# Kernel tuning notes

Hardware: AMD Instinct MI355X
Metric: run time of the kernel (lower is better)

## Reference

```python
import jax, jax.numpy as jnp
import numpy as np

B, CQ, CK, CV, CO = 16, 256, 256, 256, 256
H, W = 80, 80          # query spatial size (P3-like)
KH, KW = 40, 40        # key/value spatial size (P4-like)
HEADS = 4
R2 = 2 * 2             # region_size ** 2
SCALE = 1.0 / np.float32(np.sqrt(CQ))


def conv1x1(x, w, b):
    # 1x1 conv == per-pixel linear map over channels
    return jnp.einsum('bchw,oc->bohw', x, w) + b[None, :, None, None]


def setup_inputs() -> dict:
    key = jax.random.key(0)
    ks = jax.random.split(key, 10)
    s = 0.05
    return {
        'query': jax.random.normal(ks[0], (B, CQ, H, W), jnp.float32),
        'key':   jax.random.normal(ks[1], (B, CK, KH, KW), jnp.float32),
        'wq': jax.random.normal(ks[2], (CQ, CQ), jnp.float32) * s,
        'bq': jax.random.normal(ks[3], (CQ,), jnp.float32) * s,
        'wk': jax.random.normal(ks[4], (CK, CK), jnp.float32) * s,
        'bk': jax.random.normal(ks[5], (CK,), jnp.float32) * s,
        'wv': jax.random.normal(ks[6], (CV, CV), jnp.float32) * s,
        'bv': jax.random.normal(ks[7], (CV,), jnp.float32) * s,
        'wo': jax.random.normal(ks[8], (CO, CV), jnp.float32) * s,
        'bo': jax.random.normal(ks[9], (CO,), jnp.float32) * s,
    }


def reference(query, key, wq, bq, wk, bk, wv, bv, wo, bo):
    # value defaults to key in the original module
    q = conv1x1(query, wq, bq)               # [B,CQ,H,W]
    k = conv1x1(key, wk, bk)                 # [B,CK,KH,KW]
    v = conv1x1(key, wv, bv)                 # [B,CV,KH,KW]

    b, cq, h, w = q.shape
    # All R2 'patches' in the source are the SAME interpolation (no offsets),
    # so compute it once; bilinear resize matches torch align_corners=False.
    ki = jax.image.resize(k, (b, k.shape[1], h, w), method='bilinear')
    vi = jax.image.resize(v, (b, v.shape[1], h, w), method='bilinear')

    q5 = q.reshape(b, HEADS, cq // HEADS, h, w)
    k5 = ki.reshape(b, HEADS, k.shape[1] // HEADS, h, w)
    v5 = vi.reshape(b, HEADS, v.shape[1] // HEADS, h, w)

    # per-region score; identical for every region patch
    score = jnp.einsum('bhcxy,bhcxy->bhxy', q5, k5) * SCALE     # [B,h,H,W]
    scores = jnp.broadcast_to(score[:, :, None], (b, HEADS, R2, h, w))
    # NOTE: original uses nn.Softmax(dim=3) -> normalizes over the H axis
    attn = jax.nn.softmax(scores, axis=3)                       # [B,h,R2,H,W]

    # out = sum over regions of attn * v (v identical across regions)
    out = jnp.einsum('bhrxy,bhcxy->bhcxy', attn, v5)            # [B,h,C/h,H,W]
    out = out.reshape(b, -1, h, w)                              # [B,CV,H,W]
    return conv1x1(out, wo, bo)                                 # [B,CO,H,W]
```

## Files before the change

### kernel.cpp

```cpp
#include <hip/hip_runtime.h>
#include <hip/hip_bf16.h>

typedef __bf16 bf16;
typedef __attribute__((ext_vector_type(4))) float f32x4;
typedef __attribute__((ext_vector_type(8))) __bf16 bf16x8;
typedef __attribute__((ext_vector_type(4))) __bf16 bf16x4;

static __device__ __forceinline__ void gl16(const void* g, void* l) {
  __builtin_amdgcn_global_load_lds((const __attribute__((address_space(1))) void*)g,
                                   (__attribute__((address_space(3))) void*)l, 16, 0, 0);
}
static __device__ __forceinline__ bf16x8 frag(const bf16* tile, int row, int kb) {
  return *(const bf16x8*)(tile + row * 64 + ((((kb) >> 3) ^ (row & 7)) << 3));
}

__global__ void wpre(const float* __restrict__ w0, const float* __restrict__ w1,
                     const float* __restrict__ w2, const float* __restrict__ w3,
                     bf16* __restrict__ dst) {
  const float* srcs[4] = {w0, w1, w2, w3};
  const float* s = srcs[blockIdx.y];
  bf16* d = dst + (size_t)blockIdx.y * 65536;
  int base = blockIdx.x * 2048 + threadIdx.x * 8;
  f32x4 a = *(const f32x4*)(s + base);
  f32x4 b = *(const f32x4*)(s + base + 4);
  bf16x8 v = {(bf16)a[0], (bf16)a[1], (bf16)a[2], (bf16)a[3],
              (bf16)b[0], (bf16)b[1], (bf16)b[2], (bf16)b[3]};
  *(bf16x8*)(d + base) = v;
}

__global__ __launch_bounds__(256, 1)
void qscore(const float* __restrict__ query, const bf16* __restrict__ Wq,
            const float* __restrict__ bq, const bf16* __restrict__ Kpm,
            float* __restrict__ score) {
  __shared__ alignas(16) char smem[64 * 264 * 2];
  const int t = threadIdx.x;
  const int b = blockIdx.z;
  const int p0 = blockIdx.x * 64;
  const int w = t >> 6, l = t & 63;
  const int lrow = l & 15, ksel = l >> 4;
  const int pq = t & 15, cq = t >> 4;
  const float* actb = query + (size_t)b * 256 * 6400;
  bf16* As = (bf16*)smem;

  f32x4 Ar[4][4];
#pragma unroll
  for (int kt = 0; kt < 4; ++kt)
#pragma unroll
    for (int j = 0; j < 4; ++j)
      Ar[kt][j] = *(const f32x4*)(actb + (size_t)(kt * 64 + cq * 4 + j) * 6400 + p0 + pq * 4);
#pragma unroll
  for (int kt = 0; kt < 4; ++kt) {
    bf16* tile = As + kt * 4096;
#pragma unroll
    for (int e = 0; e < 4; ++e) {
      int row = pq * 4 + e;
      bf16x4 v = {(bf16)Ar[kt][0][e], (bf16)Ar[kt][1][e], (bf16)Ar[kt][2][e], (bf16)Ar[kt][3][e]};
      *(bf16x4*)(tile + row * 64 + ((((cq >> 1) ^ (row & 7)) << 3) | ((cq & 1) << 2))) = v;
    }
  }
  __syncthreads();

  f32x4 acc[4][4];
#pragma unroll
  for (int i = 0; i < 4; ++i)
#pragma unroll
    for (int j = 0; j < 4; ++j) acc[i][j] = (f32x4){0.f, 0.f, 0.f, 0.f};

#pragma unroll
  for (int kt = 0; kt < 4; ++kt) {
    const int k0 = kt * 64;
    const bf16* tile = As + kt * 4096;
    bf16x8 af[4][2], bv[4][2];
#pragma unroll
    for (int mi = 0; mi < 4; ++mi)
#pragma unroll
      for (int kk = 0; kk < 2; ++kk)
        af[mi][kk] = *(const bf16x8*)(Wq + (size_t)(w * 64 + mi * 16 + lrow) * 256 +
                                      k0 + kk * 32 + ksel * 8);
#pragma unroll
    for (int ni = 0; ni < 4; ++ni)
#pragma unroll
      for (int kk = 0; kk < 2; ++kk)
        bv[ni][kk] = frag(tile, ni * 16 + lrow, kk * 32 + ksel * 8);
#pragma unroll
    for (int kk = 0; kk < 2; ++kk)
#pragma unroll
      for (int mi = 0; mi < 4; ++mi)
#pragma unroll
        for (int ni = 0; ni < 4; ++ni)
          acc[mi][ni] = __builtin_amdgcn_mfma_f32_16x16x32_bf16(af[mi][kk], bv[ni][kk],
                                                                acc[mi][ni], 0, 0, 0);
  }
  __syncthreads();

  bf16* Qs = (bf16*)smem;
#pragma unroll
  for (int mi = 0; mi < 4; ++mi) {
#pragma unroll
    for (int r = 0; r < 4; ++r) {
      int o = w * 64 + mi * 16 + ksel * 4 + r;
      float bvf = bq[o];
#pragma unroll
      for (int ni = 0; ni < 4; ++ni) {
        int px = ni * 16 + lrow;
        Qs[px * 264 + o] = (bf16)(acc[mi][ni][r] + bvf);
      }
    }
  }
  __syncthreads();

  {
    int pl = t & 63, hd = t >> 6;
    int p = p0 + pl;
    int x = p / 80, y = p % 80;
    float cx = 0.5f * x - 0.25f;
    int ix = (int)floorf(cx);
    float wx1 = cx - ix;
    int x0 = ix < 0 ? 0 : ix, x1 = (ix + 1 > 39) ? 39 : ix + 1;
    float cy = 0.5f * y - 0.25f;
    int iy = (int)floorf(cy);
    float wy1 = cy - iy;
    int y0 = iy < 0 ? 0 : iy, y1 = (iy + 1 > 39) ? 39 : iy + 1;
    float w00 = (1.f - wx1) * (1.f - wy1), w01 = (1.f - wx1) * wy1;
    float w10 = wx1 * (1.f - wy1), w11 = wx1 * wy1;
    const bf16* k00 = Kpm + ((size_t)b * 1600 + x0 * 40 + y0) * 256 + hd * 64;
    const bf16* k01 = Kpm + ((size_t)b * 1600 + x0 * 40 + y1) * 256 + hd * 64;
    const bf16* k10 = Kpm + ((size_t)b * 1600 + x1 * 40 + y0) * 256 + hd * 64;
    const bf16* k11 = Kpm + ((size_t)b * 1600 + x1 * 40 + y1) * 256 + hd * 64;
    float dot = 0.f;
#pragma unroll
    for (int i = 0; i < 8; ++i) {
      bf16x8 qv = *(const bf16x8*)(Qs + pl * 264 + hd * 64 + i * 8);
      bf16x8 a = *(const bf16x8*)(k00 + i * 8);
      bf16x8 c = *(const bf16x8*)(k01 + i * 8);
      bf16x8 d = *(const bf16x8*)(k10 + i * 8);
      bf16x8 e = *(const bf16x8*)(k11 + i * 8);
#pragma unroll
      for (int j = 0; j < 8; ++j) {
        float kup = w00 * (float)a[j] + w01 * (float)c[j] + w10 * (float)d[j] + w11 * (float)e[j];
        dot += (float)qv[j] * kup;
      }
    }
    score[((size_t)b * 4 + hd) * 6400 + p] = dot * 0.0625f;
  }
}

__global__ __launch_bounds__(256, 1)
void kv_proj(const float* __restrict__ key,
             const bf16* __restrict__ Wk, const float* __restrict__ bk, bf16* __restrict__ Kpm,
             const bf16* __restrict__ Wv, const float* __restrict__ bv, bf16* __restrict__ Vpm) {
  __shared__ alignas(16) char smem[64 * 264 * 2];
  const int P = 1600;
  const int t = threadIdx.x;
  const int b = blockIdx.z;
  const int p0 = blockIdx.x * 64;
  const int sel = blockIdx.y;
  const bf16* W = sel ? Wv : Wk;
  const float* bias = sel ? bv : bk;
  bf16* out = sel ? Vpm : Kpm;
  const int w = t >> 6, l = t & 63;
  const int lrow = l & 15, ksel = l >> 4;
  const int pq = t & 15, cq = t >> 4;
  const float* actb = key + (size_t)b * 256 * P;
  bf16* As = (bf16*)smem;

  f32x4 Ar[4][4];
#pragma unroll
  for (int kt = 0; kt < 4; ++kt)
#pragma unroll
    for (int j = 0; j < 4; ++j)
      Ar[kt][j] = *(const f32x4*)(actb + (size_t)(kt * 64 + cq * 4 + j) * P + p0 + pq * 4);
#pragma unroll
  for (int kt = 0; kt < 4; ++kt) {
    bf16* tile = As + kt * 4096;
#pragma unroll
    for (int e = 0; e < 4; ++e) {
      int row = pq * 4 + e;
      bf16x4 v = {(bf16)Ar[kt][0][e], (bf16)Ar[kt][1][e], (bf16)Ar[kt][2][e], (bf16)Ar[kt][3][e]};
      *(bf16x4*)(tile + row * 64 + ((((cq >> 1) ^ (row & 7)) << 3) | ((cq & 1) << 2))) = v;
    }
  }
  __syncthreads();

  f32x4 acc[4][4];
#pragma unroll
  for (int i = 0; i < 4; ++i)
#pragma unroll
    for (int j = 0; j < 4; ++j) acc[i][j] = (f32x4){0.f, 0.f, 0.f, 0.f};

#pragma unroll
  for (int kt = 0; kt < 4; ++kt) {
    const int k0 = kt * 64;
    const bf16* tile = As + kt * 4096;
    bf16x8 af[4][2], bv8[4][2];
#pragma unroll
    for (int mi = 0; mi < 4; ++mi)
#pragma unroll
      for (int kk = 0; kk < 2; ++kk)
        af[mi][kk] = *(const bf16x8*)(W + (size_t)(w * 64 + mi * 16 + lrow) * 256 +
                                      k0 + kk * 32 + ksel * 8);
#pragma unroll
    for (int ni = 0; ni < 4; ++ni)
#pragma unroll
      for (int kk = 0; kk < 2; ++kk)
        bv8[ni][kk] = frag(tile, ni * 16 + lrow, kk * 32 + ksel * 8);
#pragma unroll
    for (int kk = 0; kk < 2; ++kk)
#pragma unroll
      for (int mi = 0; mi < 4; ++mi)
#pragma unroll
        for (int ni = 0; ni < 4; ++ni)
          acc[mi][ni] = __builtin_amdgcn_mfma_f32_16x16x32_bf16(af[mi][kk], bv8[ni][kk],
                                                                acc[mi][ni], 0, 0, 0);
  }
  __syncthreads();

  bf16* Sc = (bf16*)smem;
#pragma unroll
  for (int mi = 0; mi < 4; ++mi) {
#pragma unroll
    for (int r = 0; r < 4; ++r) {
      int o = w * 64 + mi * 16 + ksel * 4 + r;
      float bvf = bias[o];
#pragma unroll
      for (int ni = 0; ni < 4; ++ni) {
        int px = ni * 16 + lrow;
        Sc[px * 264 + o] = (bf16)(acc[mi][ni][r] + bvf);
      }
    }
  }
  __syncthreads();
  bf16* ob = out + (size_t)b * P * 256 + (size_t)p0 * 256;
#pragma unroll
  for (int pass = 0; pass < 8; ++pass) {
    int idx = pass * 256 + t;
    int row = idx >> 5, cu = idx & 31;
    bf16x8 v = *(const bf16x8*)(Sc + row * 264 + cu * 8);
    *(bf16x8*)(ob + (size_t)row * 256 + cu * 8) = v;
  }
}

__global__ void smax_kernel(float* __restrict__ score) {
  __shared__ float s[6400];
  const int hd = blockIdx.x, b = blockIdx.y, t = threadIdx.x;
  float* buf = score + ((size_t)b * 4 + hd) * 6400;
  for (int i = t; i < 6400; i += 256) s[i] = buf[i];
  __syncthreads();
  if (t < 80) {
    const int y = t;
    float m = -1e30f;
    for (int x = 0; x < 80; ++x) m = fmaxf(m, s[x * 80 + y]);
    float sum = 0.f;
    for (int x = 0; x < 80; ++x) {
      float e = __expf(s[x * 80 + y] - m);
      s[x * 80 + y] = e;
      sum += e;
    }
    float inv = 4.0f / sum;
    for (int x = 0; x < 80; ++x) buf[x * 80 + y] = s[x * 80 + y] * inv;
  }
}

__global__ __launch_bounds__(256, 4)
void uv_gemm(const bf16* __restrict__ Vpm, const bf16* __restrict__ Wo,
             bf16* __restrict__ Uv) {
  __shared__ alignas(16) bf16 Vt[64 * 64];
  const int t = threadIdx.x;
  const int b = blockIdx.z;
  const int hd = blockIdx.y;
  const int q0 = blockIdx.x * 64;
  const int w = t >> 6, l = t & 63;
  const int lrow = l & 15, ksel = l >> 4;

  const bf16* vsrc = Vpm + ((size_t)b * 1600 + q0) * 256 + hd * 64;
#pragma unroll
  for (int call = 0; call < 2; ++call) {
    int idx = (w * 2 + call) * 64 + l;
    int q = idx >> 3, u = idx & 7;
    gl16(vsrc + (size_t)q * 256 + ((u ^ (q & 7)) << 3), Vt + idx * 8);
  }
  asm volatile("s_waitcnt vmcnt(0)" ::: "memory");
  __syncthreads();

  f32x4 acc[4][4];
#pragma unroll
  for (int i = 0; i < 4; ++i)
#pragma unroll
    for (int j = 0; j < 4; ++j) acc[i][j] = (f32x4){0.f, 0.f, 0.f, 0.f};

#pragma unroll
  for (int kk = 0; kk < 2; ++kk) {
    bf16x8 af[4], bv[4];
#pragma unroll
    for (int mi = 0; mi < 4; ++mi)
      af[mi] = *(const bf16x8*)(Wo + (size_t)(w * 64 + mi * 16 + lrow) * 256 +
                                hd * 64 + kk * 32 + ksel * 8);
#pragma unroll
    for (int ni = 0; ni < 4; ++ni)
      bv[ni] = frag(Vt, ni * 16 + lrow, kk * 32 + ksel * 8);
#pragma unroll
    for (int mi = 0; mi < 4; ++mi)
#pragma unroll
      for (int ni = 0; ni < 4; ++ni)
        acc[mi][ni] = __builtin_amdgcn_mfma_f32_16x16x32_bf16(af[mi], bv[ni], acc[mi][ni], 0, 0, 0);
  }

  bf16* ob = Uv + ((size_t)(b * 4 + hd)) * 256 * 1600;
#pragma unroll
  for (int mi = 0; mi < 4; ++mi) {
#pragma unroll
    for (int ni = 0; ni < 4; ++ni) {
#pragma unroll
      for (int r = 0; r < 4; ++r) {
        int o = w * 64 + mi * 16 + ksel * 4 + r;
        int q = q0 + ni * 16 + lrow;
        ob[(size_t)o * 1600 + q] = (bf16)acc[mi][ni][r];
      }
    }
  }
}

__global__ __launch_bounds__(256, 8)
void combine(const bf16* __restrict__ Uv, const float* __restrict__ attn,
             const float* __restrict__ bo, float* __restrict__ out) {
  __shared__ bf16 Us[4][1600];
  __shared__ int   sx0[80], sx1[80];
  __shared__ float swx[80];
  const int t = threadIdx.x;
  const int o = blockIdx.x;
  const int b = blockIdx.y;

  const bf16* usrc = Uv + (size_t)(b * 4) * 256 * 1600 + (size_t)o * 1600;
  for (int idx = t; idx < 800; idx += 256) {
    int hd = idx / 200, u = idx % 200;
    *(bf16x8*)&Us[hd][u * 8] = *(const bf16x8*)(usrc + (size_t)hd * 256 * 1600 + u * 8);
  }
  if (t < 80) {
    float c = 0.5f * t - 0.25f;
    int i0 = (int)floorf(c);
    swx[t] = c - i0;
    sx0[t] = i0 < 0 ? 0 : i0;
    sx1[t] = (i0 + 1 > 39) ? 39 : i0 + 1;
  }
  __syncthreads();

  const float bias = bo[o];
  const float* attb = attn + (size_t)b * 4 * 6400;
  float* op = out + ((size_t)b * 256 + o) * 6400;

  for (int p = t; p < 6400; p += 256) {
    int x = p / 80, y = p - x * 80;
    int x0 = sx0[x], x1 = sx1[x], y0 = sx0[y], y1 = sx1[y];
    float wx1 = swx[x], wy1 = swx[y];
    float w00 = (1.f - wx1) * (1.f - wy1), w01 = (1.f - wx1) * wy1;
    float w10 = wx1 * (1.f - wy1), w11 = wx1 * wy1;
    int q00 = x0 * 40 + y0, q01 = x0 * 40 + y1, q10 = x1 * 40 + y0, q11 = x1 * 40 + y1;
    float acc = bias;
#pragma unroll
    for (int hd = 0; hd < 4; ++hd) {
      float up = w00 * (float)Us[hd][q00] + w01 * (float)Us[hd][q01] +
                 w10 * (float)Us[hd][q10] + w11 * (float)Us[hd][q11];
      acc += attb[hd * 6400 + p] * up;
    }
    op[p] = acc;
  }
}

extern "C" void kernel_launch(void* const* d_in, const int* in_sizes, int n_in,
                              void* d_out, int out_size, void* d_ws, size_t ws_size,
                              hipStream_t stream) {
  const float* query = (const float*)d_in[0];
  const float* key   = (const float*)d_in[1];
  const float* wq    = (const float*)d_in[2];
  const float* bq    = (const float*)d_in[3];
  const float* wk    = (const float*)d_in[4];
  const float* bk    = (const float*)d_in[5];
  const float* wv    = (const float*)d_in[6];
  const float* bv    = (const float*)d_in[7];
  const float* wo    = (const float*)d_in[8];
  const float* bo    = (const float*)d_in[9];

  char* ws = (char*)d_ws;
  bf16*  Uv    = (bf16*)(ws);
  bf16*  Kpm   = (bf16*)(ws + 52428800);
  bf16*  Vpm   = (bf16*)(ws + 65536000);
  float* score = (float*)(ws + 78643200);
  bf16*  Wb    = (bf16*)(ws + 85196800);
  bf16* wqb = Wb, *wkb = Wb + 65536, *wvb = Wb + 131072, *wob = Wb + 196608;

  wpre<<<dim3(32, 4), 256, 0, stream>>>(wq, wk, wv, wo, Wb);
  kv_proj<<<dim3(25, 2, 16), 256, 0, stream>>>(key, wkb, bk, Kpm, wvb, bv, Vpm);
  qscore<<<dim3(100, 1, 16), 256, 0, stream>>>(query, wqb, bq, Kpm, score);
  smax_kernel<<<dim3(4, 16), 256, 0, stream>>>(score);
  uv_gemm<<<dim3(25, 4, 16), 256, 0, stream>>>(Vpm, wob, Uv);
  combine<<<dim3(256, 16), 256, 0, stream>>>(Uv, score, bo, (float*)d_out);
}
```

Measured before the change: 179.9 us.

## Reassociate query score to project keys through Wq instead of projecting queries

Instead of projecting all 6400 query pixels through Wq and then dotting with upsampled keys, the score is rewritten as query·(Wq^T·K_h) plus bq·K_h. A transposed Wq is multiplied with the 1600-pixel key map, reusing the uv_gemm kernel. A new streaming kernel then reads the raw query and bilinearly interpolates the precomputed per-head key projections, avoiding the large Q GEMM at 6400 pixels. This adds per-head intermediates of 256×1600 per batch, stores temporaries in the output buffer, and computes bilinear taps inside the inner loop.

```diff
diff --git a/kernel.cpp b/kernel.cpp
--- a/kernel.cpp
+++ b/kernel.cpp
@@ -28,120 +28,21 @@
   *(bf16x8*)(d + base) = v;
 }
 
-__global__ __launch_bounds__(256, 1)
-void qscore(const float* __restrict__ query, const bf16* __restrict__ Wq,
-            const float* __restrict__ bq, const bf16* __restrict__ Kpm,
-            float* __restrict__ score) {
-  __shared__ alignas(16) char smem[64 * 264 * 2];
-  const int t = threadIdx.x;
-  const int b = blockIdx.z;
-  const int p0 = blockIdx.x * 64;
-  const int w = t >> 6, l = t & 63;
-  const int lrow = l & 15, ksel = l >> 4;
-  const int pq = t & 15, cq = t >> 4;
-  const float* actb = query + (size_t)b * 256 * 6400;
-  bf16* As = (bf16*)smem;
-
-  f32x4 Ar[4][4];
-#pragma unroll
-  for (int kt = 0; kt < 4; ++kt)
-#pragma unroll
-    for (int j = 0; j < 4; ++j)
-      Ar[kt][j] = *(const f32x4*)(actb + (size_t)(kt * 64 + cq * 4 + j) * 6400 + p0 + pq * 4);
-#pragma unroll
-  for (int kt = 0; kt < 4; ++kt) {
-    bf16* tile = As + kt * 4096;
-#pragma unroll
-    for (int e = 0; e < 4; ++e) {
-      int row = pq * 4 + e;
-      bf16x4 v = {(bf16)Ar[kt][0][e], (bf16)Ar[kt][1][e], (bf16)Ar[kt][2][e], (bf16)Ar[kt][3][e]};
-      *(bf16x4*)(tile + row * 64 + ((((cq >> 1) ^ (row & 7)) << 3) | ((cq & 1) << 2))) = v;
-    }
-  }
-  __syncthreads();
-
-  f32x4 acc[4][4];
-#pragma unroll
-  for (int i = 0; i < 4; ++i)
-#pragma unroll
-    for (int j = 0; j < 4; ++j) acc[i][j] = (f32x4){0.f, 0.f, 0.f, 0.f};
-
-#pragma unroll
-  for (int kt = 0; kt < 4; ++kt) {
-    const int k0 = kt * 64;
-    const bf16* tile = As + kt * 4096;
-    bf16x8 af[4][2], bv[4][2];
-#pragma unroll
-    for (int mi = 0; mi < 4; ++mi)
-#pragma unroll
-      for (int kk = 0; kk < 2; ++kk)
-        af[mi][kk] = *(const bf16x8*)(Wq + (size_t)(w * 64 + mi * 16 + lrow) * 256 +
-                                      k0 + kk * 32 + ksel * 8);
-#pragma unroll
-    for (int ni = 0; ni < 4; ++ni)
-#pragma unroll
-      for (int kk = 0; kk < 2; ++kk)
-        bv[ni][kk] = frag(tile, ni * 16 + lrow, kk * 32 + ksel * 8);
-#pragma unroll
-    for (int kk = 0; kk < 2; ++kk)
-#pragma unroll
-      for (int mi = 0; mi < 4; ++mi)
-#pragma unroll
-        for (int ni = 0; ni < 4; ++ni)
-          acc[mi][ni] = __builtin_amdgcn_mfma_f32_16x16x32_bf16(af[mi][kk], bv[ni][kk],
-                                                                acc[mi][ni], 0, 0, 0);
-  }
-  __syncthreads();
-
-  bf16* Qs = (bf16*)smem;
-#pragma unroll
-  for (int mi = 0; mi < 4; ++mi) {
-#pragma unroll
-    for (int r = 0; r < 4; ++r) {
-      int o = w * 64 + mi * 16 + ksel * 4 + r;
-      float bvf = bq[o];
-#pragma unroll
-      for (int ni = 0; ni < 4; ++ni) {
-        int px = ni * 16 + lrow;
-        Qs[px * 264 + o] = (bf16)(acc[mi][ni][r] + bvf);
-      }
-    }
-  }
-  __syncthreads();
-
-  {
-    int pl = t & 63, hd = t >> 6;
-    int p = p0 + pl;
-    int x = p / 80, y = p % 80;
-    float cx = 0.5f * x - 0.25f;
-    int ix = (int)floorf(cx);
-    float wx1 = cx - ix;
-    int x0 = ix < 0 ? 0 : ix, x1 = (ix + 1 > 39) ? 39 : ix + 1;
-    float cy = 0.5f * y - 0.25f;
-    int iy = (int)floorf(cy);
-    float wy1 = cy - iy;
-    int y0 = iy < 0 ? 0 : iy, y1 = (iy + 1 > 39) ? 39 : iy + 1;
-    float w00 = (1.f - wx1) * (1.f - wy1), w01 = (1.f - wx1) * wy1;
-    float w10 = wx1 * (1.f - wy1), w11 = wx1 * wy1;
-    const bf16* k00 = Kpm + ((size_t)b * 1600 + x0 * 40 + y0) * 256 + hd * 64;
-    const bf16* k01 = Kpm + ((size_t)b * 1600 + x0 * 40 + y1) * 256 + hd * 64;
-    const bf16* k10 = Kpm + ((size_t)b * 1600 + x1 * 40 + y0) * 256 + hd * 64;
-    const bf16* k11 = Kpm + ((size_t)b * 1600 + x1 * 40 + y1) * 256 + hd * 64;
-    float dot = 0.f;
-#pragma unroll
-    for (int i = 0; i < 8; ++i) {
-      bf16x8 qv = *(const bf16x8*)(Qs + pl * 264 + hd * 64 + i * 8);
-      bf16x8 a = *(const bf16x8*)(k00 + i * 8);
-      bf16x8 c = *(const bf16x8*)(k01 + i * 8);
-      bf16x8 d = *(const bf16x8*)(k10 + i * 8);
-      bf16x8 e = *(const bf16x8*)(k11 + i * 8);
-#pragma unroll
-      for (int j = 0; j < 8; ++j) {
-        float kup = w00 * (float)a[j] + w01 * (float)c[j] + w10 * (float)d[j] + w11 * (float)e[j];
-        dot += (float)qv[j] * kup;
-      }
-    }
-    score[((size_t)b * 4 + hd) * 6400 + p] = dot * 0.0625f;
+__global__ void wtr(const float* __restrict__ wq, bf16* __restrict__ wqT) {
+  __shared__ float tl[64][65];
+  const int r0 = blockIdx.x * 64, c0 = blockIdx.y * 64;
+  const int t = threadIdx.x;
+  const int cc = t & 63, rr = t >> 6;
+#pragma unroll
+  for (int i = 0; i < 16; ++i) {
+    int r = i * 4 + rr;
+    tl[r][cc] = wq[(size_t)(r0 + r) * 256 + c0 + cc];
+  }
+  __syncthreads();
+#pragma unroll
+  for (int i = 0; i < 16; ++i) {
+    int r = i * 4 + rr;
+    wqT[(size_t)(c0 + r) * 256 + r0 + cc] = (bf16)tl[cc][r];
   }
 }
 
@@ -240,6 +141,171 @@
   }
 }
 
+__global__ __launch_bounds__(256, 4)
+void uv_gemm(const bf16* __restrict__ Bpm, const bf16* __restrict__ A,
+             bf16* __restrict__ D) {
+  __shared__ alignas(16) bf16 Vt[64 * 64];
+  const int t = threadIdx.x;
+  const int b = blockIdx.z;
+  const int hd = blockIdx.y;
+  const int q0 = blockIdx.x * 64;
+  const int w = t >> 6, l = t & 63;
+  const int lrow = l & 15, ksel = l >> 4;
+
+  const bf16* vsrc = Bpm + ((size_t)b * 1600 + q0) * 256 + hd * 64;
+#pragma unroll
+  for (int call = 0; call < 2; ++call) {
+    int idx = (w * 2 + call) * 64 + l;
+    int q = idx >> 3, u = idx & 7;
+    gl16(vsrc + (size_t)q * 256 + ((u ^ (q & 7)) << 3), Vt + idx * 8);
+  }
+  asm volatile("s_waitcnt vmcnt(0)" ::: "memory");
+  __syncthreads();
+
+  f32x4 acc[4][4];
+#pragma unroll
+  for (int i = 0; i < 4; ++i)
+#pragma unroll
+    for (int j = 0; j < 4; ++j) acc[i][j] = (f32x4){0.f, 0.f, 0.f, 0.f};
+
+#pragma unroll
+  for (int kk = 0; kk < 2; ++kk) {
+    bf16x8 af[4], bv[4];
+#pragma unroll
+    for (int mi = 0; mi < 4; ++mi)
+      af[mi] = *(const bf16x8*)(A + (size_t)(w * 64 + mi * 16 + lrow) * 256 +
+                                hd * 64 + kk * 32 + ksel * 8);
+#pragma unroll
+    for (int ni = 0; ni < 4; ++ni)
+      bv[ni] = frag(Vt, ni * 16 + lrow, kk * 32 + ksel * 8);
+#pragma unroll
+    for (int mi = 0; mi < 4; ++mi)
+#pragma unroll
+      for (int ni = 0; ni < 4; ++ni)
+        acc[mi][ni] = __builtin_amdgcn_mfma_f32_16x16x32_bf16(af[mi], bv[ni], acc[mi][ni], 0, 0, 0);
+  }
+
+  bf16* ob = D + ((size_t)(b * 4 + hd)) * 256 * 1600;
+#pragma unroll
+  for (int mi = 0; mi < 4; ++mi) {
+#pragma unroll
+    for (int ni = 0; ni < 4; ++ni) {
+#pragma unroll
+      for (int r = 0; r < 4; ++r) {
+        int o = w * 64 + mi * 16 + ksel * 4 + r;
+        int q = q0 + ni * 16 + lrow;
+        ob[(size_t)o * 1600 + q] = (bf16)acc[mi][ni][r];
+      }
+    }
+  }
+}
+
+__global__ void beta_k(const bf16* __restrict__ Kpm, const float* __restrict__ bq,
+                       bf16* __restrict__ beta) {
+  __shared__ float bqs[256];
+  const int t = threadIdx.x;
+  bqs[t] = bq[t];
+  __syncthreads();
+  const int b = blockIdx.y;
+  const int q = blockIdx.x * 64 + (t >> 2);
+  const int hd = t & 3;
+  const bf16* row = Kpm + ((size_t)b * 1600 + q) * 256 + hd * 64;
+  float s = 0.f;
+#pragma unroll
+  for (int i = 0; i < 8; ++i) {
+    bf16x8 v = *(const bf16x8*)(row + i * 8);
+#pragma unroll
+    for (int j = 0; j < 8; ++j) s += (float)v[j] * bqs[hd * 64 + i * 8 + j];
+  }
+  beta[((size_t)b * 4 + hd) * 1600 + q] = (bf16)s;
+}
+
+__global__ __launch_bounds__(256, 3)
+void stream_score(const float* __restrict__ query, const bf16* __restrict__ T,
+                  const bf16* __restrict__ beta, float* __restrict__ score) {
+  __shared__ alignas(16) bf16 Tc[2][64][192];
+  __shared__ bf16 Bs[4][192];
+  const int t = threadIdx.x;
+  const int p0 = blockIdx.x * 256;
+  const int b = blockIdx.y;
+  const int px = p0 + t;
+  const int x = px / 80, y = px % 80;
+
+  const int x_min = p0 / 80;
+  int ixm = (int)floorf(0.5f * x_min - 0.25f);
+  int xr0 = ixm < 0 ? 0 : ixm;
+  int qbase = xr0 * 40;
+  if (qbase > 1408) qbase = 1408;
+
+  float cx = 0.5f * x - 0.25f;
+  int ix = (int)floorf(cx);
+  float wx1 = cx - ix;
+  int x0 = ix < 0 ? 0 : ix, x1 = (ix + 1 > 39) ? 39 : ix + 1;
+  float cy = 0.5f * y - 0.25f;
+  int iy = (int)floorf(cy);
+  float wy1 = cy - iy;
+  int y0 = iy < 0 ? 0 : iy, y1 = (iy + 1 > 39) ? 39 : iy + 1;
+  const float w00 = (1.f - wx1) * (1.f - wy1), w01 = (1.f - wx1) * wy1;
+  const float w10 = wx1 * (1.f - wy1), w11 = wx1 * wy1;
+  const int r00 = x0 * 40 + y0 - qbase, r01 = x0 * 40 + y1 - qbase;
+  const int r10 = x1 * 40 + y0 - qbase, r11 = x1 * 40 + y1 - qbase;
+
+  for (int i = t; i < 768; i += 256) {
+    int hd = i / 192, qq = i - hd * 192;
+    Bs[hd][qq] = beta[((size_t)b * 4 + hd) * 1600 + qbase + qq];
+  }
+
+  const bf16* Tb = T + (size_t)b * 4 * 256 * 1600;
+
+  auto STAGE = [&](int c, int buf) {
+    const int k0 = c * 16;
+#pragma unroll
+    for (int call = 0; call < 6; ++call) {
+      int idx = call * 256 + t;
+      int r = idx / 24, u = idx - r * 24;
+      int hd = r >> 4, kk = r & 15;
+      const bf16* src = Tb + ((size_t)(hd * 256) + k0 + kk) * 1600 + qbase + u * 8;
+      gl16(src, &Tc[buf][0][0] + idx * 8);
+    }
+  };
+
+  STAGE(0, 0);
+  asm volatile("s_waitcnt vmcnt(0)" ::: "memory");
+  __syncthreads();
+
+  float acc[4];
+#pragma unroll
+  for (int hd = 0; hd < 4; ++hd)
+    acc[hd] = w00 * (float)Bs[hd][r00] + w01 * (float)Bs[hd][r01] +
+              w10 * (float)Bs[hd][r10] + w11 * (float)Bs[hd][r11];
+
+  int buf = 0;
+  for (int c = 0; c < 16; ++c) {
+    if (c < 15) STAGE(c + 1, buf ^ 1);
+    float qv[16];
+#pragma unroll
+    for (int kk = 0; kk < 16; ++kk)
+      qv[kk] = query[((size_t)b * 256 + c * 16 + kk) * 6400 + px];
+#pragma unroll
+    for (int kk = 0; kk < 16; ++kk) {
+#pragma unroll
+      for (int hd = 0; hd < 4; ++hd) {
+        const bf16* row = &Tc[buf][hd * 16 + kk][0];
+        float tv = w00 * (float)row[r00] + w01 * (float)row[r01] +
+                   w10 * (float)row[r10] + w11 * (float)row[r11];
+        acc[hd] += qv[kk] * tv;
+      }
+    }
+    asm volatile("s_waitcnt vmcnt(0)" ::: "memory");
+    __syncthreads();
+    buf ^= 1;
+  }
+
+#pragma unroll
+  for (int hd = 0; hd < 4; ++hd)
+    score[((size_t)b * 4 + hd) * 6400 + px] = 0.0625f * acc[hd];
+}
+
 __global__ void smax_kernel(float* __restrict__ score) {
   __shared__ float s[6400];
   const int hd = blockIdx.x, b = blockIdx.y, t = threadIdx.x;
@@ -258,65 +324,6 @@
     }
     float inv = 4.0f / sum;
     for (int x = 0; x < 80; ++x) buf[x * 80 + y] = s[x * 80 + y] * inv;
-  }
-}
-
-__global__ __launch_bounds__(256, 4)
-void uv_gemm(const bf16* __restrict__ Vpm, const bf16* __restrict__ Wo,
-             bf16* __restrict__ Uv) {
-  __shared__ alignas(16) bf16 Vt[64 * 64];
-  const int t = threadIdx.x;
-  const int b = blockIdx.z;
-  const int hd = blockIdx.y;
-  const int q0 = blockIdx.x * 64;
-  const int w = t >> 6, l = t & 63;
-  const int lrow = l & 15, ksel = l >> 4;
-
-  const bf16* vsrc = Vpm + ((size_t)b * 1600 + q0) * 256 + hd * 64;
-#pragma unroll
-  for (int call = 0; call < 2; ++call) {
-    int idx = (w * 2 + call) * 64 + l;
-    int q = idx >> 3, u = idx & 7;
-    gl16(vsrc + (size_t)q * 256 + ((u ^ (q & 7)) << 3), Vt + idx * 8);
-  }
-  asm volatile("s_waitcnt vmcnt(0)" ::: "memory");
-  __syncthreads();
-
-  f32x4 acc[4][4];
-#pragma unroll
-  for (int i = 0; i < 4; ++i)
-#pragma unroll
-    for (int j = 0; j < 4; ++j) acc[i][j] = (f32x4){0.f, 0.f, 0.f, 0.f};
-
-#pragma unroll
-  for (int kk = 0; kk < 2; ++kk) {
-    bf16x8 af[4], bv[4];
-#pragma unroll
-    for (int mi = 0; mi < 4; ++mi)
-      af[mi] = *(const bf16x8*)(Wo + (size_t)(w * 64 + mi * 16 + lrow) * 256 +
-                                hd * 64 + kk * 32 + ksel * 8);
-#pragma unroll
-    for (int ni = 0; ni < 4; ++ni)
-      bv[ni] = frag(Vt, ni * 16 + lrow, kk * 32 + ksel * 8);
-#pragma unroll
-    for (int mi = 0; mi < 4; ++mi)
-#pragma unroll
-      for (int ni = 0; ni < 4; ++ni)
-        acc[mi][ni] = __builtin_amdgcn_mfma_f32_16x16x32_bf16(af[mi], bv[ni], acc[mi][ni], 0, 0, 0);
-  }
-
-  bf16* ob = Uv + ((size_t)(b * 4 + hd)) * 256 * 1600;
-#pragma unroll
-  for (int mi = 0; mi < 4; ++mi) {
-#pragma unroll
-    for (int ni = 0; ni < 4; ++ni) {
-#pragma unroll
-      for (int r = 0; r < 4; ++r) {
-        int o = w * 64 + mi * 16 + ksel * 4 + r;
-        int q = q0 + ni * 16 + lrow;
-        ob[(size_t)o * 1600 + q] = (bf16)acc[mi][ni][r];
-      }
-    }
   }
 }
 
@@ -381,16 +388,23 @@
   const float* bo    = (const float*)d_in[9];
 
   char* ws = (char*)d_ws;
+  bf16*  T     = (bf16*)(ws);
   bf16*  Uv    = (bf16*)(ws);
   bf16*  Kpm   = (bf16*)(ws + 52428800);
   bf16*  Vpm   = (bf16*)(ws + 65536000);
   float* score = (float*)(ws + 78643200);
   bf16*  Wb    = (bf16*)(ws + 85196800);
   bf16* wqb = Wb, *wkb = Wb + 65536, *wvb = Wb + 131072, *wob = Wb + 196608;
+  (void)wqb;
+  bf16*  wqT   = (bf16*)d_out;
+  bf16*  beta  = (bf16*)((char*)d_out + 131072);
 
   wpre<<<dim3(32, 4), 256, 0, stream>>>(wq, wk, wv, wo, Wb);
+  wtr<<<dim3(4, 4), 256, 0, stream>>>(wq, wqT);
   kv_proj<<<dim3(25, 2, 16), 256, 0, stream>>>(key, wkb, bk, Kpm, wvb, bv, Vpm);
-  qscore<<<dim3(100, 1, 16), 256, 0, stream>>>(query, wqb, bq, Kpm, score);
+  uv_gemm<<<dim3(25, 4, 16), 256, 0, stream>>>(Kpm, wqT, T);
+  beta_k<<<dim3(25, 16), 256, 0, stream>>>(Kpm, bq, beta);
+  stream_score<<<dim3(25, 16), 256, 0, stream>>>(query, T, beta, score);
   smax_kernel<<<dim3(4, 16), 256, 0, stream>>>(score);
   uv_gemm<<<dim3(25, 4, 16), 256, 0, stream>>>(Vpm, wob, Uv);
   combine<<<dim3(256, 16), 256, 0, stream>>>(Uv, score, bo, (float*)d_out);
```

Result: slower. 207.6 us (+15.4%).
